# Kernel tuning notes

Measured on AMD Instinct MI355X. Metric: run time of the kernel, lower is better.

Reference implementation:

```python
import jax, jax.numpy as jnp
import numpy as np

N_EMB = 512
N_HEADS = 8
HEAD_SIZE = N_EMB // N_HEADS  # 64
B, T = 4, 2048
EPS = 1e-5


def layernorm(x, g, b):
    mu = jnp.mean(x, axis=-1, keepdims=True)
    var = jnp.var(x, axis=-1, keepdims=True)
    return (x - mu) * jax.lax.rsqrt(var + EPS) * g + b


def setup_inputs() -> dict:
    key = jax.random.key(0)
    ks = jax.random.split(key, 8)
    s = 1.0 / np.sqrt(N_EMB)
    x = jax.random.normal(ks[0], (B, T, N_EMB), dtype=jnp.float32)
    # per-head q/k/v weights stacked: [H, n_emb, head_size]
    wq = jax.random.uniform(ks[1], (N_HEADS, N_EMB, HEAD_SIZE), minval=-s, maxval=s, dtype=jnp.float32)
    wk = jax.random.uniform(ks[2], (N_HEADS, N_EMB, HEAD_SIZE), minval=-s, maxval=s, dtype=jnp.float32)
    wv = jax.random.uniform(ks[3], (N_HEADS, N_EMB, HEAD_SIZE), minval=-s, maxval=s, dtype=jnp.float32)
    w_ff = jax.random.uniform(ks[4], (N_EMB, N_EMB), minval=-s, maxval=s, dtype=jnp.float32)
    b_ff = jax.random.uniform(ks[5], (N_EMB,), minval=-s, maxval=s, dtype=jnp.float32)
    ln1_g = jnp.ones((N_EMB,), jnp.float32)
    ln1_b = jnp.zeros((N_EMB,), jnp.float32)
    ln2_g = jnp.ones((N_EMB,), jnp.float32)
    ln2_b = jnp.zeros((N_EMB,), jnp.float32)
    return {"x": x, "wq": wq, "wk": wk, "wv": wv, "w_ff": w_ff, "b_ff": b_ff,
            "ln1_g": ln1_g, "ln1_b": ln1_b, "ln2_g": ln2_g, "ln2_b": ln2_b}


def reference(x, wq, wk, wv, w_ff, b_ff, ln1_g, ln1_b, ln2_g, ln2_b):
    # --- self-attention branch (dropout=0 -> identity) ---
    h = layernorm(x, ln1_g, ln1_b)                       # [B,T,C]
    q = jnp.einsum('btc,hcd->bhtd', h, wq)               # [B,H,T,d]
    k = jnp.einsum('btc,hcd->bhtd', h, wk)
    v = jnp.einsum('btc,hcd->bhtd', h, wv)
    scale = HEAD_SIZE ** -0.5
    wei = jnp.einsum('bhtd,bhsd->bhts', q, k) * scale    # [B,H,T,T]
    Tt = x.shape[1]
    causal = jnp.tril(jnp.ones((Tt, Tt), dtype=bool))
    wei = jnp.where(causal, wei, -jnp.inf)
    wei = jax.nn.softmax(wei, axis=-1)
    attn = jnp.einsum('bhts,bhsd->bhtd', wei, v)         # [B,H,T,d]
    # concat heads along last dim (head order preserved)
    Bn, H, Tn, d = attn.shape
    sa = jnp.transpose(attn, (0, 2, 1, 3)).reshape(Bn, Tn, H * d)
    x = x + sa
    # --- feed-forward branch: Linear + ReLU (dropout=0) ---
    h2 = layernorm(x, ln2_g, ln2_b)
    ff = jax.nn.relu(h2 @ w_ff + b_ff)
    return x + ff
```

## Files before the change

kernel.cpp:

```cpp
#include <hip/hip_runtime.h>

#define Bsz  4
#define Tseq 2048
#define Cdim 512
#define Hn   8
#define Dh   64
#define BT   8192
#define NQKV 1536
#define NEG_BIG (-1e30f)

typedef __attribute__((ext_vector_type(8))) short bf16x8;
typedef __attribute__((ext_vector_type(4))) short bf16x4;
typedef __attribute__((ext_vector_type(4))) float f32x4;

__device__ __forceinline__ float b2f(short s) {
    unsigned u = ((unsigned)(unsigned short)s) << 16;
    float f; __builtin_memcpy(&f, &u, 4); return f;
}
__device__ __forceinline__ short f2b(float f) {
    unsigned u; __builtin_memcpy(&u, &f, 4);
    u = (u + 0x7fffu + ((u >> 16) & 1u)) >> 16;
    return (short)u;
}
__device__ __forceinline__ void g2l16(const short* g, short* l) {
    __builtin_amdgcn_global_load_lds(
        (const __attribute__((address_space(1))) unsigned int*)(uintptr_t)g,
        (__attribute__((address_space(3))) unsigned int*)l, 16, 0, 0);
}

__global__ __launch_bounds__(256) void k_prep(const float* __restrict__ wq, const float* __restrict__ wk,
                                              const float* __restrict__ wv, const float* __restrict__ wff,
                                              short* __restrict__ wqkvt, short* __restrict__ wfft,
                                              const float* __restrict__ x, const float* __restrict__ g,
                                              const float* __restrict__ b, short* __restrict__ out) {
    const int blk = blockIdx.x, tid = threadIdx.x;
    if (blk < 256) {
        __shared__ float ldsT[64 * 65];
        if (blk < 192) {
            int hm = blk >> 3, ct = blk & 7;
            int proj = hm >> 3, h = hm & 7;
            const float* w = (proj == 0) ? wq : (proj == 1 ? wk : wv);
#pragma unroll
            for (int i = 0; i < 16; i++) {
                int flat = i * 256 + tid, cc = flat >> 6, dd = flat & 63;
                ldsT[dd * 65 + cc] = w[(h * 512 + ct * 64 + cc) * 64 + dd];
            }
            __syncthreads();
#pragma unroll
            for (int i = 0; i < 16; i++) {
                int flat = i * 256 + tid, dd = flat >> 6, cc = flat & 63;
                int n = proj * 512 + h * 64 + dd;
                wqkvt[n * 512 + ct * 64 + cc] = f2b(ldsT[dd * 65 + cc]);
            }
        } else {
            int b2 = blk - 192, rt = b2 >> 3, nt8 = b2 & 7;
#pragma unroll
            for (int i = 0; i < 16; i++) {
                int flat = i * 256 + tid, cc = flat >> 6, nn = flat & 63;
                ldsT[nn * 65 + cc] = wff[(rt * 64 + cc) * 512 + nt8 * 64 + nn];
            }
            __syncthreads();
#pragma unroll
            for (int i = 0; i < 16; i++) {
                int flat = i * 256 + tid, nn = flat >> 6, cc = flat & 63;
                wfft[(nt8 * 64 + nn) * 512 + rt * 64 + cc] = f2b(ldsT[nn * 65 + cc]);
            }
        }
    } else {
        int row  = (blk - 256) * 4 + (tid >> 6);
        int lane = tid & 63;
        const f32x4 a0 = *(const f32x4*)(x + row * Cdim + lane * 8);
        const f32x4 a1 = *(const f32x4*)(x + row * Cdim + lane * 8 + 4);
        float v[8] = {a0[0], a0[1], a0[2], a0[3], a1[0], a1[1], a1[2], a1[3]};
        float s = 0.f, sq = 0.f;
#pragma unroll
        for (int i = 0; i < 8; i++) { s += v[i]; sq += v[i] * v[i]; }
#pragma unroll
        for (int off = 1; off < 64; off <<= 1) { s += __shfl_xor(s, off); sq += __shfl_xor(sq, off); }
        float mean = s * (1.f / 512.f);
        float var  = sq * (1.f / 512.f) - mean * mean;
        float rstd = rsqrtf(var + 1e-5f);
        const f32x4 g0 = *(const f32x4*)(g + lane * 8);
        const f32x4 g1 = *(const f32x4*)(g + lane * 8 + 4);
        const f32x4 b0 = *(const f32x4*)(b + lane * 8);
        const f32x4 b1 = *(const f32x4*)(b + lane * 8 + 4);
        float gg[8] = {g0[0], g0[1], g0[2], g0[3], g1[0], g1[1], g1[2], g1[3]};
        float bb[8] = {b0[0], b0[1], b0[2], b0[3], b1[0], b1[1], b1[2], b1[3]};
        bf16x8 o;
#pragma unroll
        for (int i = 0; i < 8; i++) o[i] = f2b((v[i] - mean) * rstd * gg[i] + bb[i]);
        *(bf16x8*)(out + row * Cdim + lane * 8) = o;
    }
}

__global__ __launch_bounds__(256) void k_ln(const float* __restrict__ x, const float* __restrict__ g,
                                            const float* __restrict__ b, short* __restrict__ out) {
    int row  = blockIdx.x * 4 + (threadIdx.x >> 6);
    int lane = threadIdx.x & 63;
    const f32x4 a0 = *(const f32x4*)(x + row * Cdim + lane * 8);
    const f32x4 a1 = *(const f32x4*)(x + row * Cdim + lane * 8 + 4);
    float v[8] = {a0[0], a0[1], a0[2], a0[3], a1[0], a1[1], a1[2], a1[3]};
    float s = 0.f, sq = 0.f;
#pragma unroll
    for (int i = 0; i < 8; i++) { s += v[i]; sq += v[i] * v[i]; }
#pragma unroll
    for (int off = 1; off < 64; off <<= 1) { s += __shfl_xor(s, off); sq += __shfl_xor(sq, off); }
    float mean = s * (1.f / 512.f);
    float var  = sq * (1.f / 512.f) - mean * mean;
    float rstd = rsqrtf(var + 1e-5f);
    const f32x4 g0 = *(const f32x4*)(g + lane * 8);
    const f32x4 g1 = *(const f32x4*)(g + lane * 8 + 4);
    const f32x4 b0 = *(const f32x4*)(b + lane * 8);
    const f32x4 b1 = *(const f32x4*)(b + lane * 8 + 4);
    float gg[8] = {g0[0], g0[1], g0[2], g0[3], g1[0], g1[1], g1[2], g1[3]};
    float bb[8] = {b0[0], b0[1], b0[2], b0[3], b1[0], b1[1], b1[2], b1[3]};
    bf16x8 o;
#pragma unroll
    for (int i = 0; i < 8; i++) o[i] = f2b((v[i] - mean) * rstd * gg[i] + bb[i]);
    *(bf16x8*)(out + row * Cdim + lane * 8) = o;
}

__global__ __launch_bounds__(256) void k_gemm_qkv(const short* __restrict__ A, const short* __restrict__ Wt,
                                                  short* __restrict__ q, short* __restrict__ k,
                                                  short* __restrict__ vt) {
    const int tid = threadIdx.x;
    const int wave = tid >> 6, lane = tid & 63;
    const int quad = lane >> 4, l15 = lane & 15;
    const int m0 = blockIdx.x * 128, n0 = blockIdx.y * 128;
    const int wm = wave & 1, wn = wave >> 1;
    __shared__ __align__(16) short As[2][128 * 32];
    __shared__ __align__(16) short Bs[2][128 * 32];
    f32x4 acc[4][4];
#pragma unroll
    for (int i = 0; i < 4; i++)
#pragma unroll
        for (int j = 0; j < 4; j++) acc[i][j] = (f32x4){0.f, 0.f, 0.f, 0.f};
    const int lr = lane >> 2, lc = lane & 3;
    const short* Ag = A  + (m0 + wave * 32 + lr) * Cdim + lc * 8;
    const short* Bg = Wt + (n0 + wave * 32 + lr) * Cdim + lc * 8;
    g2l16(Ag,             &As[0][wave * 1024]);
    g2l16(Ag + 16 * Cdim, &As[0][wave * 1024 + 512]);
    g2l16(Bg,             &Bs[0][wave * 1024]);
    g2l16(Bg + 16 * Cdim, &Bs[0][wave * 1024 + 512]);
    __syncthreads();
    for (int kk = 0; kk < 16; kk++) {
        const int cur = kk & 1, nxt = cur ^ 1;
        if (kk + 1 < 16) {
            const int k0 = (kk + 1) * 32;
            g2l16(Ag + k0,             &As[nxt][wave * 1024]);
            g2l16(Ag + 16 * Cdim + k0, &As[nxt][wave * 1024 + 512]);
            g2l16(Bg + k0,             &Bs[nxt][wave * 1024]);
            g2l16(Bg + 16 * Cdim + k0, &Bs[nxt][wave * 1024 + 512]);
        }
        bf16x8 a[4], w[4];
#pragma unroll
        for (int mt = 0; mt < 4; mt++) a[mt] = *(const bf16x8*)(&As[cur][(wm * 64 + mt * 16 + l15) * 32 + quad * 8]);
#pragma unroll
        for (int nt = 0; nt < 4; nt++) w[nt] = *(const bf16x8*)(&Bs[cur][(wn * 64 + nt * 16 + l15) * 32 + quad * 8]);
#pragma unroll
        for (int mt = 0; mt < 4; mt++)
#pragma unroll
            for (int nt = 0; nt < 4; nt++)
                acc[mt][nt] = __builtin_amdgcn_mfma_f32_16x16x32_bf16(a[mt], w[nt], acc[mt][nt], 0, 0, 0);
        __syncthreads();
    }
    const int proj = n0 >> 9;
    const int n0w  = n0 + wn * 64;
    const int hh   = (n0w & 511) >> 6;
    const int m0w  = m0 + wm * 64;
#pragma unroll
    for (int mt = 0; mt < 4; mt++) {
#pragma unroll
        for (int r = 0; r < 4; r++) {
            int t  = m0w + mt * 16 + quad * 4 + r;
            int bi = t >> 11, tt = t & 2047;
#pragma unroll
            for (int nt = 0; nt < 4; nt++) {
                int d = nt * 16 + l15;
                short val = f2b(acc[mt][nt][r]);
                if (proj == 0)      q [((bi * Hn + hh) * Tseq + tt) * Dh + d] = val;
                else if (proj == 1) k [((bi * Hn + hh) * Tseq + tt) * Dh + d] = val;
                else                vt[((bi * Hn + hh) * Dh + d) * Tseq + tt] = val;
            }
        }
    }
}

__global__ __launch_bounds__(256, 3) void k_attn(const short* __restrict__ qb, const short* __restrict__ kb,
                                                 const short* __restrict__ vtb, const float* __restrict__ x,
                                                 float* __restrict__ out1) {
    const int wave = threadIdx.x >> 6, lane = threadIdx.x & 63;
    const int quad = lane >> 4, l15 = lane & 15;
    const int D  = blockIdx.y * 32 + blockIdx.x;
    const int j5 = D & 31;
    const int bh = (j5 & 7) * 4 + (j5 >> 3);
    const int u  = D >> 5, kq = u >> 3, d8 = u & 7;
    const int qg = (kq == 0) ? 31 - d8 : (kq == 1) ? 16 + d8 : (kq == 2) ? 15 - d8 : d8;
    const int q0  = qg * 64;
    const int qw0 = q0 + wave * 16;
    const int nkt = qg + 1;

    const short* Q = qb  + bh * Tseq * Dh;
    const short* K = kb  + bh * Tseq * Dh;
    const short* V = vtb + bh * Dh * Tseq;

    __shared__ __align__(16) short Ks[2][64 * 64];
    __shared__ __align__(16) short Vs[2][64 * 64];
    __shared__ __align__(16) short Ps[4][16 * 72];
    short* pw = &Ps[wave][0];

    const int lr8 = lane >> 3, lc8 = lane & 7;
    const int sw8 = (lc8 ^ lr8) << 3;
    const short* Ksrc = K + (wave * 16 + lr8) * Dh + sw8;
    const short* Vsrc = V + (wave * 16 + lr8) * Tseq + sw8;

    g2l16(Ksrc,            &Ks[0][wave * 1024]);
    g2l16(Ksrc + 8 * Dh,   &Ks[0][wave * 1024 + 512]);
    g2l16(Vsrc,            &Vs[0][wave * 1024]);
    g2l16(Vsrc + 8 * Tseq, &Vs[0][wave * 1024 + 512]);

    bf16x8 qa[2];
#pragma unroll
    for (int c = 0; c < 2; c++)
        qa[c] = *(const bf16x8*)(Q + (qw0 + l15) * Dh + c * 32 + quad * 8);

    f32x4 o[4];
#pragma unroll
    for (int i = 0; i < 4; i++) o[i] = (f32x4){0.f, 0.f, 0.f, 0.f};
    float m_i = NEG_BIG, l_i = 0.f;

    const float sc = 0.125f * 1.44269504089f;
    const int sx = l15 & 7;

    __syncthreads();

    for (int kt = 0; kt < nkt; kt++) {
        const short* Kb = &Ks[kt & 1][0];
        const short* Vb = &Vs[kt & 1][0];
        if (kt + 1 < nkt) {
            g2l16(Ksrc + (kt + 1) * 64 * Dh,            &Ks[(kt + 1) & 1][wave * 1024]);
            g2l16(Ksrc + (kt + 1) * 64 * Dh + 8 * Dh,   &Ks[(kt + 1) & 1][wave * 1024 + 512]);
            g2l16(Vsrc + (kt + 1) * 64,                 &Vs[(kt + 1) & 1][wave * 1024]);
            g2l16(Vsrc + (kt + 1) * 64 + 8 * Tseq,      &Vs[(kt + 1) & 1][wave * 1024 + 512]);
        }
        const int s0 = kt * 64;
        f32x4 st[4];
#pragma unroll
        for (int nt = 0; nt < 4; nt++) {
            bf16x8 k0 = *(const bf16x8*)(Kb + (nt * 16 + l15) * 64 + ((quad ^ sx) << 3));
            bf16x8 k1 = *(const bf16x8*)(Kb + (nt * 16 + l15) * 64 + (((4 | quad) ^ sx) << 3));
            f32x4 z = (f32x4){0.f, 0.f, 0.f, 0.f};
            z = __builtin_amdgcn_mfma_f32_16x16x32_bf16(k0, qa[0], z, 0, 0, 0);
            z = __builtin_amdgcn_mfma_f32_16x16x32_bf16(k1, qa[1], z, 0, 0, 0);
            st[nt] = z;
        }
        const int qq = qw0 + l15;
        if (kt == nkt - 1) {
#pragma unroll
            for (int nt = 0; nt < 4; nt++)
#pragma unroll
                for (int r = 0; r < 4; r++) {
                    int s = s0 + nt * 16 + quad * 4 + r;
                    st[nt][r] = (s > qq) ? NEG_BIG : st[nt][r] * sc;
                }
        } else {
#pragma unroll
            for (int nt = 0; nt < 4; nt++)
#pragma unroll
                for (int r = 0; r < 4; r++) st[nt][r] *= sc;
        }
        float mx = fmaxf(fmaxf(fmaxf(st[0][0], st[0][1]), fmaxf(st[0][2], st[0][3])),
                         fmaxf(fmaxf(st[1][0], st[1][1]), fmaxf(st[1][2], st[1][3])));
        mx = fmaxf(mx, fmaxf(fmaxf(fmaxf(st[2][0], st[2][1]), fmaxf(st[2][2], st[2][3])),
                             fmaxf(fmaxf(st[3][0], st[3][1]), fmaxf(st[3][2], st[3][3]))));
        mx = fmaxf(mx, __shfl_xor(mx, 16));
        mx = fmaxf(mx, __shfl_xor(mx, 32));
        float mn    = fmaxf(m_i, mx);
        float alpha = __builtin_amdgcn_exp2f(m_i - mn);
        m_i = mn;
        float rs = 0.f;
        bf16x4 pk[4];
#pragma unroll
        for (int nt = 0; nt < 4; nt++) {
#pragma unroll
            for (int r = 0; r < 4; r++) {
                float p = __builtin_amdgcn_exp2f(st[nt][r] - mn);
                rs += p;
                pk[nt][r] = f2b(p);
            }
        }
        rs += __shfl_xor(rs, 16);
        rs += __shfl_xor(rs, 32);
        l_i = l_i * alpha + rs;
#pragma unroll
        for (int nt = 0; nt < 4; nt++)
            *(bf16x4*)(pw + l15 * 72 + nt * 16 + quad * 4) = pk[nt];
#pragma unroll
        for (int r = 0; r < 4; r++) {
            float ar = __shfl(alpha, quad * 4 + r);
#pragma unroll
            for (int dt = 0; dt < 4; dt++) o[dt][r] *= ar;
        }
        asm volatile("s_waitcnt lgkmcnt(0)" ::: "memory");
        bf16x8 pa[2];
#pragma unroll
        for (int c = 0; c < 2; c++)
            pa[c] = *(const bf16x8*)(pw + l15 * 72 + c * 32 + quad * 8);
#pragma unroll
        for (int c = 0; c < 2; c++)
#pragma unroll
            for (int v4 = 0; v4 < 4; v4++) {
                bf16x8 vb = *(const bf16x8*)(Vb + (v4 * 16 + l15) * 64 + ((((c << 2) | quad) ^ sx) << 3));
                o[v4] = __builtin_amdgcn_mfma_f32_16x16x32_bf16(pa[c], vb, o[v4], 0, 0, 0);
            }
        __syncthreads();
    }
    const int bi = bh >> 3, hh = bh & 7;
#pragma unroll
    for (int r = 0; r < 4; r++) {
        int row = quad * 4 + r;
        float Lr  = __shfl(l_i, row);
        float inv = 1.f / Lr;
#pragma unroll
        for (int v4 = 0; v4 < 4; v4++) {
            int t   = qw0 + row;
            int idx = (bi * Tseq + t) * Cdim + hh * Dh + v4 * 16 + l15;
            out1[idx] = x[idx] + o[v4][r] * inv;
        }
    }
}

__global__ __launch_bounds__(256) void k_gemm_ff(const short* __restrict__ A, const short* __restrict__ Wt,
                                                 const float* __restrict__ bias, const float* __restrict__ res,
                                                 float* __restrict__ out) {
    const int tid = threadIdx.x;
    const int wave = tid >> 6, lane = tid & 63;
    const int quad = lane >> 4, l15 = lane & 15;
    const int m0 = blockIdx.x * 128, n0 = blockIdx.y * 64;
    const int wm = wave & 1, wn = wave >> 1;
    __shared__ __align__(16) short As[2][128 * 32];
    __shared__ __align__(16) short Bs[2][64 * 32];
    f32x4 acc[4][2];
#pragma unroll
    for (int i = 0; i < 4; i++)
#pragma unroll
        for (int j = 0; j < 2; j++) acc[i][j] = (f32x4){0.f, 0.f, 0.f, 0.f};
    const int lr = lane >> 2, lc = lane & 3;
    const short* Ag = A  + (m0 + wave * 32 + lr) * Cdim + lc * 8;
    const short* Bg = Wt + (n0 + wave * 16 + lr) * Cdim + lc * 8;
    g2l16(Ag,             &As[0][wave * 1024]);
    g2l16(Ag + 16 * Cdim, &As[0][wave * 1024 + 512]);
    g2l16(Bg,             &Bs[0][wave * 512]);
    __syncthreads();
    for (int kk = 0; kk < 16; kk++) {
        const int cur = kk & 1, nxt = cur ^ 1;
        if (kk + 1 < 16) {
            const int k0 = (kk + 1) * 32;
            g2l16(Ag + k0,             &As[nxt][wave * 1024]);
            g2l16(Ag + 16 * Cdim + k0, &As[nxt][wave * 1024 + 512]);
            g2l16(Bg + k0,             &Bs[nxt][wave * 512]);
        }
        bf16x8 a[4], w[2];
#pragma unroll
        for (int mt = 0; mt < 4; mt++) a[mt] = *(const bf16x8*)(&As[cur][(wm * 64 + mt * 16 + l15) * 32 + quad * 8]);
#pragma unroll
        for (int nt = 0; nt < 2; nt++) w[nt] = *(const bf16x8*)(&Bs[cur][(wn * 32 + nt * 16 + l15) * 32 + quad * 8]);
#pragma unroll
        for (int mt = 0; mt < 4; mt++)
#pragma unroll
            for (int nt = 0; nt < 2; nt++)
                acc[mt][nt] = __builtin_amdgcn_mfma_f32_16x16x32_bf16(a[mt], w[nt], acc[mt][nt], 0, 0, 0);
        __syncthreads();
    }
    const int m0w = m0 + wm * 64, n0w = n0 + wn * 32;
#pragma unroll
    for (int mt = 0; mt < 4; mt++) {
#pragma unroll
        for (int r = 0; r < 4; r++) {
            int t = m0w + mt * 16 + quad * 4 + r;
#pragma unroll
            for (int nt = 0; nt < 2; nt++) {
                int n = n0w + nt * 16 + l15;
                float fv = acc[mt][nt][r] + bias[n];
                fv = fmaxf(fv, 0.f);
                out[t * Cdim + n] = res[t * Cdim + n] + fv;
            }
        }
    }
}

extern "C" void kernel_launch(void* const* d_in, const int* in_sizes, int n_in,
                              void* d_out, int out_size, void* d_ws, size_t ws_size,
                              hipStream_t stream) {
    const float* x   = (const float*)d_in[0];
    const float* wq  = (const float*)d_in[1];
    const float* wk  = (const float*)d_in[2];
    const float* wv  = (const float*)d_in[3];
    const float* wff = (const float*)d_in[4];
    const float* bff = (const float*)d_in[5];
    const float* g1  = (const float*)d_in[6];
    const float* b1  = (const float*)d_in[7];
    const float* g2  = (const float*)d_in[8];
    const float* b2  = (const float*)d_in[9];

    char* p = (char*)d_ws;
    short* wqkvt = (short*)p; p += (size_t)NQKV * Cdim * 2;
    short* wfft  = (short*)p; p += (size_t)Cdim * Cdim * 2;
    short* h1    = (short*)p; p += (size_t)BT * Cdim * 2;
    short* qb    = (short*)p; p += (size_t)BT * Cdim * 2;
    short* kb    = (short*)p; p += (size_t)BT * Cdim * 2;
    short* vtb   = (short*)p; p += (size_t)BT * Cdim * 2;
    float* out1  = (float*)p; p += (size_t)BT * Cdim * 4;

    hipLaunchKernelGGL(k_prep,     dim3(2304),    dim3(256), 0, stream,
                       wq, wk, wv, wff, wqkvt, wfft, x, g1, b1, h1);
    hipLaunchKernelGGL(k_gemm_qkv, dim3(64, 12),  dim3(256), 0, stream, h1, wqkvt, qb, kb, vtb);
    hipLaunchKernelGGL(k_attn,     dim3(32, 32),  dim3(256), 0, stream, qb, kb, vtb, x, out1);
    hipLaunchKernelGGL(k_ln,       dim3(2048),    dim3(256), 0, stream, out1, g2, b2, h1);
    hipLaunchKernelGGL(k_gemm_ff,  dim3(64, 8),   dim3(256), 0, stream, h1, wfft, bff, out1, (float*)d_out);
}
```

Baseline: 172.9 us.

## Process two 64-row query tiles per attention block to reuse K/V tiles

Each attention block now handles 128 query rows, split into two 64-row sub-tiles A and B that share each K/V tile loaded into LDS. The grid is halved and the last diagonal tile is peeled so that only sub-tile B processes it. The aim is to halve K/V global-to-LDS traffic and barrier count per unit of work. In exchange, register pressure roughly doubles under launch_bounds(256,3), there are fewer blocks to fill the GPU, and the causal load balance across blocks becomes coarser.

```diff
diff --git a/kernel.cpp b/kernel.cpp
--- a/kernel.cpp
+++ b/kernel.cpp
@@ -194,11 +194,12 @@
     const int D  = blockIdx.y * 32 + blockIdx.x;
     const int j5 = D & 31;
     const int bh = (j5 & 7) * 4 + (j5 >> 3);
-    const int u  = D >> 5, kq = u >> 3, d8 = u & 7;
-    const int qg = (kq == 0) ? 31 - d8 : (kq == 1) ? 16 + d8 : (kq == 2) ? 15 - d8 : d8;
-    const int q0  = qg * 64;
-    const int qw0 = q0 + wave * 16;
-    const int nkt = qg + 1;
+    const int u  = D >> 5;
+    const int qg = (u < 8) ? 15 - u : u - 8;
+    const int q0  = qg * 128;
+    const int qA0 = q0 + wave * 16;
+    const int qB0 = q0 + 64 + wave * 16;
+    const int nkt = 2 * qg + 2;
 
     const short* Q = qb  + bh * Tseq * Dh;
     const short* K = kb  + bh * Tseq * Dh;
@@ -206,8 +207,9 @@
 
     __shared__ __align__(16) short Ks[2][64 * 64];
     __shared__ __align__(16) short Vs[2][64 * 64];
-    __shared__ __align__(16) short Ps[4][16 * 72];
-    short* pw = &Ps[wave][0];
+    __shared__ __align__(16) short Ps[8][16 * 72];
+    short* pwA = &Ps[wave][0];
+    short* pwB = &Ps[4 + wave][0];
 
     const int lr8 = lane >> 3, lc8 = lane & 7;
     const int sw8 = (lc8 ^ lr8) << 3;
@@ -219,113 +221,222 @@
     g2l16(Vsrc,            &Vs[0][wave * 1024]);
     g2l16(Vsrc + 8 * Tseq, &Vs[0][wave * 1024 + 512]);
 
-    bf16x8 qa[2];
-#pragma unroll
-    for (int c = 0; c < 2; c++)
-        qa[c] = *(const bf16x8*)(Q + (qw0 + l15) * Dh + c * 32 + quad * 8);
-
-    f32x4 o[4];
-#pragma unroll
-    for (int i = 0; i < 4; i++) o[i] = (f32x4){0.f, 0.f, 0.f, 0.f};
-    float m_i = NEG_BIG, l_i = 0.f;
+    bf16x8 qaA[2], qaB[2];
+#pragma unroll
+    for (int c = 0; c < 2; c++) {
+        qaA[c] = *(const bf16x8*)(Q + (qA0 + l15) * Dh + c * 32 + quad * 8);
+        qaB[c] = *(const bf16x8*)(Q + (qB0 + l15) * Dh + c * 32 + quad * 8);
+    }
+
+    f32x4 oA[4], oB[4];
+#pragma unroll
+    for (int i = 0; i < 4; i++) { oA[i] = (f32x4){0.f, 0.f, 0.f, 0.f}; oB[i] = (f32x4){0.f, 0.f, 0.f, 0.f}; }
+    float mA = NEG_BIG, lA = 0.f, mB = NEG_BIG, lB = 0.f;
 
     const float sc = 0.125f * 1.44269504089f;
     const int sx = l15 & 7;
+    const int qqA = qA0 + l15, qqB = qB0 + l15;
 
     __syncthreads();
 
-    for (int kt = 0; kt < nkt; kt++) {
+    for (int kt = 0; kt < nkt - 1; kt++) {
         const short* Kb = &Ks[kt & 1][0];
         const short* Vb = &Vs[kt & 1][0];
-        if (kt + 1 < nkt) {
-            g2l16(Ksrc + (kt + 1) * 64 * Dh,            &Ks[(kt + 1) & 1][wave * 1024]);
-            g2l16(Ksrc + (kt + 1) * 64 * Dh + 8 * Dh,   &Ks[(kt + 1) & 1][wave * 1024 + 512]);
-            g2l16(Vsrc + (kt + 1) * 64,                 &Vs[(kt + 1) & 1][wave * 1024]);
-            g2l16(Vsrc + (kt + 1) * 64 + 8 * Tseq,      &Vs[(kt + 1) & 1][wave * 1024 + 512]);
-        }
+        g2l16(Ksrc + (kt + 1) * 64 * Dh,            &Ks[(kt + 1) & 1][wave * 1024]);
+        g2l16(Ksrc + (kt + 1) * 64 * Dh + 8 * Dh,   &Ks[(kt + 1) & 1][wave * 1024 + 512]);
+        g2l16(Vsrc + (kt + 1) * 64,                 &Vs[(kt + 1) & 1][wave * 1024]);
+        g2l16(Vsrc + (kt + 1) * 64 + 8 * Tseq,      &Vs[(kt + 1) & 1][wave * 1024 + 512]);
         const int s0 = kt * 64;
-        f32x4 st[4];
+        f32x4 stA[4], stB[4];
 #pragma unroll
         for (int nt = 0; nt < 4; nt++) {
             bf16x8 k0 = *(const bf16x8*)(Kb + (nt * 16 + l15) * 64 + ((quad ^ sx) << 3));
             bf16x8 k1 = *(const bf16x8*)(Kb + (nt * 16 + l15) * 64 + (((4 | quad) ^ sx) << 3));
-            f32x4 z = (f32x4){0.f, 0.f, 0.f, 0.f};
-            z = __builtin_amdgcn_mfma_f32_16x16x32_bf16(k0, qa[0], z, 0, 0, 0);
-            z = __builtin_amdgcn_mfma_f32_16x16x32_bf16(k1, qa[1], z, 0, 0, 0);
-            st[nt] = z;
-        }
-        const int qq = qw0 + l15;
-        if (kt == nkt - 1) {
+            f32x4 zA = (f32x4){0.f, 0.f, 0.f, 0.f};
+            zA = __builtin_amdgcn_mfma_f32_16x16x32_bf16(k0, qaA[0], zA, 0, 0, 0);
+            zA = __builtin_amdgcn_mfma_f32_16x16x32_bf16(k1, qaA[1], zA, 0, 0, 0);
+            stA[nt] = zA;
+            f32x4 zB = (f32x4){0.f, 0.f, 0.f, 0.f};
+            zB = __builtin_amdgcn_mfma_f32_16x16x32_bf16(k0, qaB[0], zB, 0, 0, 0);
+            zB = __builtin_amdgcn_mfma_f32_16x16x32_bf16(k1, qaB[1], zB, 0, 0, 0);
+            stB[nt] = zB;
+        }
+        if (kt == nkt - 2) {
 #pragma unroll
             for (int nt = 0; nt < 4; nt++)
 #pragma unroll
                 for (int r = 0; r < 4; r++) {
                     int s = s0 + nt * 16 + quad * 4 + r;
-                    st[nt][r] = (s > qq) ? NEG_BIG : st[nt][r] * sc;
+                    stA[nt][r] = (s > qqA) ? NEG_BIG : stA[nt][r] * sc;
                 }
         } else {
 #pragma unroll
             for (int nt = 0; nt < 4; nt++)
 #pragma unroll
-                for (int r = 0; r < 4; r++) st[nt][r] *= sc;
-        }
-        float mx = fmaxf(fmaxf(fmaxf(st[0][0], st[0][1]), fmaxf(st[0][2], st[0][3])),
-                         fmaxf(fmaxf(st[1][0], st[1][1]), fmaxf(st[1][2], st[1][3])));
-        mx = fmaxf(mx, fmaxf(fmaxf(fmaxf(st[2][0], st[2][1]), fmaxf(st[2][2], st[2][3])),
-                             fmaxf(fmaxf(st[3][0], st[3][1]), fmaxf(st[3][2], st[3][3]))));
-        mx = fmaxf(mx, __shfl_xor(mx, 16));
-        mx = fmaxf(mx, __shfl_xor(mx, 32));
-        float mn    = fmaxf(m_i, mx);
-        float alpha = __builtin_amdgcn_exp2f(m_i - mn);
-        m_i = mn;
-        float rs = 0.f;
-        bf16x4 pk[4];
+                for (int r = 0; r < 4; r++) stA[nt][r] *= sc;
+        }
+#pragma unroll
+        for (int nt = 0; nt < 4; nt++)
+#pragma unroll
+            for (int r = 0; r < 4; r++) stB[nt][r] *= sc;
+        float mxA = fmaxf(fmaxf(fmaxf(stA[0][0], stA[0][1]), fmaxf(stA[0][2], stA[0][3])),
+                          fmaxf(fmaxf(stA[1][0], stA[1][1]), fmaxf(stA[1][2], stA[1][3])));
+        mxA = fmaxf(mxA, fmaxf(fmaxf(fmaxf(stA[2][0], stA[2][1]), fmaxf(stA[2][2], stA[2][3])),
+                               fmaxf(fmaxf(stA[3][0], stA[3][1]), fmaxf(stA[3][2], stA[3][3]))));
+        mxA = fmaxf(mxA, __shfl_xor(mxA, 16));
+        mxA = fmaxf(mxA, __shfl_xor(mxA, 32));
+        float mnA    = fmaxf(mA, mxA);
+        float alphaA = __builtin_amdgcn_exp2f(mA - mnA);
+        mA = mnA;
+        float rsA = 0.f;
+        bf16x4 pkA[4];
 #pragma unroll
         for (int nt = 0; nt < 4; nt++) {
 #pragma unroll
             for (int r = 0; r < 4; r++) {
-                float p = __builtin_amdgcn_exp2f(st[nt][r] - mn);
-                rs += p;
-                pk[nt][r] = f2b(p);
-            }
-        }
-        rs += __shfl_xor(rs, 16);
-        rs += __shfl_xor(rs, 32);
-        l_i = l_i * alpha + rs;
+                float p = __builtin_amdgcn_exp2f(stA[nt][r] - mnA);
+                rsA += p;
+                pkA[nt][r] = f2b(p);
+            }
+        }
+        rsA += __shfl_xor(rsA, 16);
+        rsA += __shfl_xor(rsA, 32);
+        lA = lA * alphaA + rsA;
 #pragma unroll
         for (int nt = 0; nt < 4; nt++)
-            *(bf16x4*)(pw + l15 * 72 + nt * 16 + quad * 4) = pk[nt];
+            *(bf16x4*)(pwA + l15 * 72 + nt * 16 + quad * 4) = pkA[nt];
+        float mxB = fmaxf(fmaxf(fmaxf(stB[0][0], stB[0][1]), fmaxf(stB[0][2], stB[0][3])),
+                          fmaxf(fmaxf(stB[1][0], stB[1][1]), fmaxf(stB[1][2], stB[1][3])));
+        mxB = fmaxf(mxB, fmaxf(fmaxf(fmaxf(stB[2][0], stB[2][1]), fmaxf(stB[2][2], stB[2][3])),
+                               fmaxf(fmaxf(stB[3][0], stB[3][1]), fmaxf(stB[3][2], stB[3][3]))));
+        mxB = fmaxf(mxB, __shfl_xor(mxB, 16));
+        mxB = fmaxf(mxB, __shfl_xor(mxB, 32));
+        float mnB    = fmaxf(mB, mxB);
+        float alphaB = __builtin_amdgcn_exp2f(mB - mnB);
+        mB = mnB;
+        float rsB = 0.f;
+        bf16x4 pkB[4];
+#pragma unroll
+        for (int nt = 0; nt < 4; nt++) {
+#pragma unroll
+            for (int r = 0; r < 4; r++) {
+                float p = __builtin_amdgcn_exp2f(stB[nt][r] - mnB);
+                rsB += p;
+                pkB[nt][r] = f2b(p);
+            }
+        }
+        rsB += __shfl_xor(rsB, 16);
+        rsB += __shfl_xor(rsB, 32);
+        lB = lB * alphaB + rsB;
+#pragma unroll
+        for (int nt = 0; nt < 4; nt++)
+            *(bf16x4*)(pwB + l15 * 72 + nt * 16 + quad * 4) = pkB[nt];
 #pragma unroll
         for (int r = 0; r < 4; r++) {
-            float ar = __shfl(alpha, quad * 4 + r);
-#pragma unroll
-            for (int dt = 0; dt < 4; dt++) o[dt][r] *= ar;
+            float arA = __shfl(alphaA, quad * 4 + r);
+            float arB = __shfl(alphaB, quad * 4 + r);
+#pragma unroll
+            for (int dt = 0; dt < 4; dt++) { oA[dt][r] *= arA; oB[dt][r] *= arB; }
         }
         asm volatile("s_waitcnt lgkmcnt(0)" ::: "memory");
-        bf16x8 pa[2];
-#pragma unroll
-        for (int c = 0; c < 2; c++)
-            pa[c] = *(const bf16x8*)(pw + l15 * 72 + c * 32 + quad * 8);
+        bf16x8 paA[2], paB[2];
+#pragma unroll
+        for (int c = 0; c < 2; c++) {
+            paA[c] = *(const bf16x8*)(pwA + l15 * 72 + c * 32 + quad * 8);
+            paB[c] = *(const bf16x8*)(pwB + l15 * 72 + c * 32 + quad * 8);
+        }
 #pragma unroll
         for (int c = 0; c < 2; c++)
 #pragma unroll
             for (int v4 = 0; v4 < 4; v4++) {
                 bf16x8 vb = *(const bf16x8*)(Vb + (v4 * 16 + l15) * 64 + ((((c << 2) | quad) ^ sx) << 3));
-                o[v4] = __builtin_amdgcn_mfma_f32_16x16x32_bf16(pa[c], vb, o[v4], 0, 0, 0);
+                oA[v4] = __builtin_amdgcn_mfma_f32_16x16x32_bf16(paA[c], vb, oA[v4], 0, 0, 0);
+                oB[v4] = __builtin_amdgcn_mfma_f32_16x16x32_bf16(paB[c], vb, oB[v4], 0, 0, 0);
             }
         __syncthreads();
+    }
+    {
+        const int kt = nkt - 1;
+        const short* Kb = &Ks[kt & 1][0];
+        const short* Vb = &Vs[kt & 1][0];
+        const int s0 = kt * 64;
+        f32x4 stB[4];
+#pragma unroll
+        for (int nt = 0; nt < 4; nt++) {
+            bf16x8 k0 = *(const bf16x8*)(Kb + (nt * 16 + l15) * 64 + ((quad ^ sx) << 3));
+            bf16x8 k1 = *(const bf16x8*)(Kb + (nt * 16 + l15) * 64 + (((4 | quad) ^ sx) << 3));
+            f32x4 zB = (f32x4){0.f, 0.f, 0.f, 0.f};
+            zB = __builtin_amdgcn_mfma_f32_16x16x32_bf16(k0, qaB[0], zB, 0, 0, 0);
+            zB = __builtin_amdgcn_mfma_f32_16x16x32_bf16(k1, qaB[1], zB, 0, 0, 0);
+            stB[nt] = zB;
+        }
+#pragma unroll
+        for (int nt = 0; nt < 4; nt++)
+#pragma unroll
+            for (int r = 0; r < 4; r++) {
+                int s = s0 + nt * 16 + quad * 4 + r;
+                stB[nt][r] = (s > qqB) ? NEG_BIG : stB[nt][r] * sc;
+            }
+        float mxB = fmaxf(fmaxf(fmaxf(stB[0][0], stB[0][1]), fmaxf(stB[0][2], stB[0][3])),
+                          fmaxf(fmaxf(stB[1][0], stB[1][1]), fmaxf(stB[1][2], stB[1][3])));
+        mxB = fmaxf(mxB, fmaxf(fmaxf(fmaxf(stB[2][0], stB[2][1]), fmaxf(stB[2][2], stB[2][3])),
+                               fmaxf(fmaxf(stB[3][0], stB[3][1]), fmaxf(stB[3][2], stB[3][3]))));
+        mxB = fmaxf(mxB, __shfl_xor(mxB, 16));
+        mxB = fmaxf(mxB, __shfl_xor(mxB, 32));
+        float mnB    = fmaxf(mB, mxB);
+        float alphaB = __builtin_amdgcn_exp2f(mB - mnB);
+        mB = mnB;
+        float rsB = 0.f;
+        bf16x4 pkB[4];
+#pragma unroll
+        for (int nt = 0; nt < 4; nt++) {
+#pragma unroll
+            for (int r = 0; r < 4; r++) {
+                float p = __builtin_amdgcn_exp2f(stB[nt][r] - mnB);
+                rsB += p;
+                pkB[nt][r] = f2b(p);
+            }
+        }
+        rsB += __shfl_xor(rsB, 16);
+        rsB += __shfl_xor(rsB, 32);
+        lB = lB * alphaB + rsB;
+#pragma unroll
+        for (int nt = 0; nt < 4; nt++)
+            *(bf16x4*)(pwB + l15 * 72 + nt * 16 + quad * 4) = pkB[nt];
+#pragma unroll
+        for (int r = 0; r < 4; r++) {
+            float arB = __shfl(alphaB, quad * 4 + r);
+#pragma unroll
+            for (int dt = 0; dt < 4; dt++) oB[dt][r] *= arB;
+        }
+        asm volatile("s_waitcnt lgkmcnt(0)" ::: "memory");
+        bf16x8 paB[2];
+#pragma unroll
+        for (int c = 0; c < 2; c++)
+            paB[c] = *(const bf16x8*)(pwB + l15 * 72 + c * 32 + quad * 8);
+#pragma unroll
+        for (int c = 0; c < 2; c++)
+#pragma unroll
+            for (int v4 = 0; v4 < 4; v4++) {
+                bf16x8 vb = *(const bf16x8*)(Vb + (v4 * 16 + l15) * 64 + ((((c << 2) | quad) ^ sx) << 3));
+                oB[v4] = __builtin_amdgcn_mfma_f32_16x16x32_bf16(paB[c], vb, oB[v4], 0, 0, 0);
+            }
     }
     const int bi = bh >> 3, hh = bh & 7;
 #pragma unroll
     for (int r = 0; r < 4; r++) {
         int row = quad * 4 + r;
-        float Lr  = __shfl(l_i, row);
-        float inv = 1.f / Lr;
+        float LrA = __shfl(lA, row);
+        float LrB = __shfl(lB, row);
+        float invA = 1.f / LrA, invB = 1.f / LrB;
 #pragma unroll
         for (int v4 = 0; v4 < 4; v4++) {
-            int t   = qw0 + row;
-            int idx = (bi * Tseq + t) * Cdim + hh * Dh + v4 * 16 + l15;
-            out1[idx] = x[idx] + o[v4][r] * inv;
+            int tA   = qA0 + row;
+            int idxA = (bi * Tseq + tA) * Cdim + hh * Dh + v4 * 16 + l15;
+            out1[idxA] = x[idxA] + oA[v4][r] * invA;
+            int tB   = qB0 + row;
+            int idxB = (bi * Tseq + tB) * Cdim + hh * Dh + v4 * 16 + l15;
+            out1[idxB] = x[idxB] + oB[v4][r] * invB;
         }
     }
 }
@@ -415,7 +526,7 @@
     hipLaunchKernelGGL(k_prep,     dim3(2304),    dim3(256), 0, stream,
                        wq, wk, wv, wff, wqkvt, wfft, x, g1, b1, h1);
     hipLaunchKernelGGL(k_gemm_qkv, dim3(64, 12),  dim3(256), 0, stream, h1, wqkvt, qb, kb, vtb);
-    hipLaunchKernelGGL(k_attn,     dim3(32, 32),  dim3(256), 0, stream, qb, kb, vtb, x, out1);
+    hipLaunchKernelGGL(k_attn,     dim3(32, 16),  dim3(256), 0, stream, qb, kb, vtb, x, out1);
     hipLaunchKernelGGL(k_ln,       dim3(2048),    dim3(256), 0, stream, out1, g2, b2, h1);
     hipLaunchKernelGGL(k_gemm_ff,  dim3(64, 8),   dim3(256), 0, stream, h1, wfft, bff, out1, (float*)d_out);
 }
```

New measurement: 192.6 us. 1.11x slower.

## Prefetch two K-tiles ahead with explicit vmcnt waits in QKV and FF GEMMs

Applied to the files above, without the earlier changes.

Both GEMM kernels now issue global-to-LDS loads for the first two K-tiles up front. Inside the loop they wait with a partial s_waitcnt vmcnt, so only the current tile must be resident and the next tile's loads stay in flight during the MFMAs. The refill of the buffer just consumed is issued after a barrier, targeting tile kk+2. This aims to hide global load latency better than the previous wait-everything __syncthreads scheme, but it depends on the exact count of outstanding vector memory ops per g2l16 and adds a second barrier per iteration.

```diff
diff --git a/kernel.cpp b/kernel.cpp
--- a/kernel.cpp
+++ b/kernel.cpp
@@ -138,20 +138,20 @@
     const int lr = lane >> 2, lc = lane & 3;
     const short* Ag = A  + (m0 + wave * 32 + lr) * Cdim + lc * 8;
     const short* Bg = Wt + (n0 + wave * 32 + lr) * Cdim + lc * 8;
-    g2l16(Ag,             &As[0][wave * 1024]);
-    g2l16(Ag + 16 * Cdim, &As[0][wave * 1024 + 512]);
-    g2l16(Bg,             &Bs[0][wave * 1024]);
-    g2l16(Bg + 16 * Cdim, &Bs[0][wave * 1024 + 512]);
-    __syncthreads();
+    g2l16(Ag,                  &As[0][wave * 1024]);
+    g2l16(Ag + 16 * Cdim,      &As[0][wave * 1024 + 512]);
+    g2l16(Bg,                  &Bs[0][wave * 1024]);
+    g2l16(Bg + 16 * Cdim,      &Bs[0][wave * 1024 + 512]);
+    g2l16(Ag + 32,             &As[1][wave * 1024]);
+    g2l16(Ag + 16 * Cdim + 32, &As[1][wave * 1024 + 512]);
+    g2l16(Bg + 32,             &Bs[1][wave * 1024]);
+    g2l16(Bg + 16 * Cdim + 32, &Bs[1][wave * 1024 + 512]);
     for (int kk = 0; kk < 16; kk++) {
-        const int cur = kk & 1, nxt = cur ^ 1;
-        if (kk + 1 < 16) {
-            const int k0 = (kk + 1) * 32;
-            g2l16(Ag + k0,             &As[nxt][wave * 1024]);
-            g2l16(Ag + 16 * Cdim + k0, &As[nxt][wave * 1024 + 512]);
-            g2l16(Bg + k0,             &Bs[nxt][wave * 1024]);
-            g2l16(Bg + 16 * Cdim + k0, &Bs[nxt][wave * 1024 + 512]);
-        }
+        const int cur = kk & 1;
+        if (kk < 15) { asm volatile("s_waitcnt vmcnt(4)" ::: "memory"); }
+        else         { asm volatile("s_waitcnt vmcnt(0)" ::: "memory"); }
+        __builtin_amdgcn_s_barrier();
+        __builtin_amdgcn_sched_barrier(0);
         bf16x8 a[4], w[4];
 #pragma unroll
         for (int mt = 0; mt < 4; mt++) a[mt] = *(const bf16x8*)(&As[cur][(wm * 64 + mt * 16 + l15) * 32 + quad * 8]);
@@ -162,7 +162,15 @@
 #pragma unroll
             for (int nt = 0; nt < 4; nt++)
                 acc[mt][nt] = __builtin_amdgcn_mfma_f32_16x16x32_bf16(a[mt], w[nt], acc[mt][nt], 0, 0, 0);
-        __syncthreads();
+        __builtin_amdgcn_sched_barrier(0);
+        __builtin_amdgcn_s_barrier();
+        if (kk + 2 < 16) {
+            const int k0 = (kk + 2) * 32;
+            g2l16(Ag + k0,             &As[cur][wave * 1024]);
+            g2l16(Ag + 16 * Cdim + k0, &As[cur][wave * 1024 + 512]);
+            g2l16(Bg + k0,             &Bs[cur][wave * 1024]);
+            g2l16(Bg + 16 * Cdim + k0, &Bs[cur][wave * 1024 + 512]);
+        }
     }
     const int proj = n0 >> 9;
     const int n0w  = n0 + wn * 64;
@@ -348,18 +356,18 @@
     const int lr = lane >> 2, lc = lane & 3;
     const short* Ag = A  + (m0 + wave * 32 + lr) * Cdim + lc * 8;
     const short* Bg = Wt + (n0 + wave * 16 + lr) * Cdim + lc * 8;
-    g2l16(Ag,             &As[0][wave * 1024]);
-    g2l16(Ag + 16 * Cdim, &As[0][wave * 1024 + 512]);
-    g2l16(Bg,             &Bs[0][wave * 512]);
-    __syncthreads();
+    g2l16(Ag,                  &As[0][wave * 1024]);
+    g2l16(Ag + 16 * Cdim,      &As[0][wave * 1024 + 512]);
+    g2l16(Bg,                  &Bs[0][wave * 512]);
+    g2l16(Ag + 32,             &As[1][wave * 1024]);
+    g2l16(Ag + 16 * Cdim + 32, &As[1][wave * 1024 + 512]);
+    g2l16(Bg + 32,             &Bs[1][wave * 512]);
     for (int kk = 0; kk < 16; kk++) {
-        const int cur = kk & 1, nxt = cur ^ 1;
-        if (kk + 1 < 16) {
-            const int k0 = (kk + 1) * 32;
-            g2l16(Ag + k0,             &As[nxt][wave * 1024]);
-            g2l16(Ag + 16 * Cdim + k0, &As[nxt][wave * 1024 + 512]);
-            g2l16(Bg + k0,             &Bs[nxt][wave * 512]);
-        }
+        const int cur = kk & 1;
+        if (kk < 15) { asm volatile("s_waitcnt vmcnt(3)" ::: "memory"); }
+        else         { asm volatile("s_waitcnt vmcnt(0)" ::: "memory"); }
+        __builtin_amdgcn_s_barrier();
+        __builtin_amdgcn_sched_barrier(0);
         bf16x8 a[4], w[2];
 #pragma unroll
         for (int mt = 0; mt < 4; mt++) a[mt] = *(const bf16x8*)(&As[cur][(wm * 64 + mt * 16 + l15) * 32 + quad * 8]);
@@ -370,7 +378,14 @@
 #pragma unroll
             for (int nt = 0; nt < 2; nt++)
                 acc[mt][nt] = __builtin_amdgcn_mfma_f32_16x16x32_bf16(a[mt], w[nt], acc[mt][nt], 0, 0, 0);
-        __syncthreads();
+        __builtin_amdgcn_sched_barrier(0);
+        __builtin_amdgcn_s_barrier();
+        if (kk + 2 < 16) {
+            const int k0 = (kk + 2) * 32;
+            g2l16(Ag + k0,             &As[cur][wave * 1024]);
+            g2l16(Ag + 16 * Cdim + k0, &As[cur][wave * 1024 + 512]);
+            g2l16(Bg + k0,             &Bs[cur][wave * 512]);
+        }
     }
     const int m0w = m0 + wm * 64, n0w = n0 + wn * 32;
 #pragma unroll
```

Result: no change. 172.2 us (-0.4%).
